# Performance work log

Measured on AMD Instinct MI355X. Metric: run time of the kernel, lower is better.

## Reference

```python
import jax, jax.numpy as jnp
import numpy as np

D_MODEL = 1024
N_HEADS = 16
N_LAYERS = 4
N_LEVELS = 8
B, T = 2, 1024
EPS = 1e-5
ADALN_K = 0.1
ADALN_C = 2.0
FMAX = float(np.finfo(np.float32).max)


def setup_inputs() -> dict:
    key = jax.random.key(0)
    ks = jax.random.split(key, 12)
    d, L = D_MODEL, N_LAYERS
    x = jax.random.normal(ks[0], (B, T, d), dtype=jnp.float32)
    # ragged lengths -> padding mask (1 valid, 0 pad), shape (b, t, 1)
    lengths = jnp.array([T, (3 * T) // 4], dtype=jnp.int32)
    m = (jnp.arange(T)[None, :] < lengths[:, None]).astype(jnp.float32)[..., None]
    l = jax.random.randint(ks[1], (B,), 0, N_LEVELS, dtype=jnp.int32)
    s = 0.02
    Wqkv = jax.random.normal(ks[2], (L, d, 3 * d), dtype=jnp.float32) * s
    Wout = jax.random.normal(ks[3], (L, d, d), dtype=jnp.float32) * s
    bout = jnp.zeros((L, d), dtype=jnp.float32)
    adaln_attn = jax.random.normal(ks[4], (L, N_LEVELS, 2 * d), dtype=jnp.float32) * s
    adaln_ffn = jax.random.normal(ks[5], (L, N_LEVELS, 2 * d), dtype=jnp.float32) * s
    W1 = jax.random.normal(ks[6], (L, d, 4 * d), dtype=jnp.float32) * s
    b1 = jnp.zeros((L, 4 * d), dtype=jnp.float32)
    W2 = jax.random.normal(ks[7], (L, 4 * d, d), dtype=jnp.float32) * s
    b2 = jnp.zeros((L, d), dtype=jnp.float32)
    return dict(x=x, m=m, l=l, Wqkv=Wqkv, Wout=Wout, bout=bout,
                adaln_attn=adaln_attn, adaln_ffn=adaln_ffn,
                W1=W1, b1=b1, W2=W2, b2=b2)


def _adaln(x, emb, l):
    # emb: (n_levels, 2d); l: (b,)
    g = emb[l][:, None, :]                      # (b, 1, 2d)
    loggamma, beta = jnp.split(g, 2, axis=-1)
    mu = jnp.mean(x, axis=-1, keepdims=True)
    var = jnp.mean((x - mu) ** 2, axis=-1, keepdims=True)
    h = (x - mu) * jax.lax.rsqrt(var + EPS)
    h = ADALN_C * (1.0 - jax.lax.stop_gradient(ADALN_K * h)) * h
    return jnp.exp(loggamma) * h + beta


def _attention(x, m, Wqkv, Wout, bout):
    b, t, d = x.shape
    h = N_HEADS
    dh = d // h
    qkv = x @ Wqkv                               # (b, t, 3d)
    q, k, v = jnp.split(qkv, 3, axis=-1)
    q = q.reshape(b, t, h, dh)
    k = k.reshape(b, t, h, dh)
    v = v.reshape(b, t, h, dh)
    e = jnp.einsum('bihd,bjhd->bijh', q, k) * (dh ** -0.5)
    kpm = m[:, None, :, :] * m[:, :, None, :]    # (b, i, j, 1)
    causal = jnp.tril(jnp.ones((t, t), dtype=kpm.dtype))[None, :, :, None]
    kpm = kpm * causal
    e = jnp.where(kpm == 0, -FMAX, e)
    a = jax.nn.softmax(e, axis=2)                # softmax over j (dim=2), matches custom softmax
    o = jnp.einsum('bijh,bjhd->bihd', a, v).reshape(b, t, d)
    o = o @ Wout + bout
    return o * m


def reference(x, m, l, Wqkv, Wout, bout, adaln_attn, adaln_ffn, W1, b1, W2, b2):
    for i in range(N_LAYERS):
        # attention sub-block (PrenormResidual with AdaLN, requires_mask=True)
        h = _adaln(x, adaln_attn[i], l) * m
        x = (x + _attention(h, m, Wqkv[i], Wout[i], bout[i])) * m
        # FFN sub-block
        h = _adaln(x, adaln_ffn[i], l) * m
        ff = jax.nn.gelu(h @ W1[i] + b1[i], approximate=False) @ W2[i] + b2[i]
        x = (x + ff) * m
    return x
```

## Files before the change

kernel.cpp:

```cpp
#include <hip/hip_runtime.h>

#define D_MODEL 1024
#define N_HEADS 16
#define DH 64
#define N_LAYERS 4
#define N_LEVELS 8
#define BB 2
#define TT 1024
#define MM (BB*TT)
#define EPSV 1e-5f

typedef float f32x4 __attribute__((ext_vector_type(4)));
typedef short bf16x8 __attribute__((ext_vector_type(8)));

__device__ __forceinline__ float bf2f(unsigned short u) {
    union { unsigned int i; float f; } c; c.i = ((unsigned int)u) << 16; return c.f;
}
__device__ __forceinline__ unsigned short f2bf(float f) {
    union { float f; unsigned int i; } c; c.f = f;
    unsigned int x = c.i;
    return (unsigned short)((x + 0x7fffu + ((x >> 16) & 1u)) >> 16);
}
__device__ __forceinline__ float cvt_in(const void* src, long long j, int isbf) {
    return isbf ? bf2f(((const unsigned short*)src)[j]) : ((const float*)src)[j];
}

__device__ __forceinline__ void gl_lds16(const unsigned short* g, unsigned short* l) {
    __builtin_amdgcn_global_load_lds(
        (const __attribute__((address_space(1))) unsigned int*)g,
        (__attribute__((address_space(3))) unsigned int*)l,
        16, 0, 0);
}

__global__ void detect_kernel(const unsigned short* __restrict__ x, int* __restrict__ flag) {
    __shared__ int cnts[256];
    int cnt = 0;
    for (int i = threadIdx.x; i < 16384; i += 256) {
        unsigned short u = x[2 * i];
        int e = (u >> 7) & 0xFF;
        if (e >= 110 && e <= 140) cnt++;
    }
    cnts[threadIdx.x] = cnt;
    __syncthreads();
    for (int s = 128; s; s >>= 1) {
        if (threadIdx.x < s) cnts[threadIdx.x] += cnts[threadIdx.x + s];
        __syncthreads();
    }
    if (threadIdx.x == 0) flag[0] = (cnts[0] > 12000) ? 1 : 0;
}

__global__ void load_f32_kernel(const void* __restrict__ src, float* __restrict__ dst,
                                const int* __restrict__ flag, int n) {
    int i = blockIdx.x * 256 + threadIdx.x;
    if (i >= n) return;
    dst[i] = cvt_in(src, i, flag[0]);
}
__global__ void load_small_kernel(const void* m_in, const void* aa, const void* af_,
                                  const void* bo, const void* b1, const void* b2,
                                  float* mf, float* embA, float* embF,
                                  float* boutf, float* b1f, float* b2f,
                                  const int* __restrict__ flag) {
    int i = blockIdx.x * 256 + threadIdx.x;
    int isbf = flag[0];
    if (i < 2048)        mf[i] = cvt_in(m_in, i, isbf);
    else if (i < 67584)  embA[i - 2048] = cvt_in(aa, i - 2048, isbf);
    else if (i < 133120) embF[i - 67584] = cvt_in(af_, i - 67584, isbf);
    else if (i < 137216) boutf[i - 133120] = cvt_in(bo, i - 133120, isbf);
    else if (i < 153600) b1f[i - 137216] = cvt_in(b1, i - 137216, isbf);
    else if (i < 157696) b2f[i - 153600] = cvt_in(b2, i - 153600, isbf);
}

__global__ __launch_bounds__(256)
void transpose_layer_kernel(const void* Wqkv, const void* Wo, const void* W1, const void* W2,
                            unsigned short* wq, unsigned short* wo,
                            unsigned short* w1, unsigned short* w2,
                            const int* __restrict__ flag,
                            long long o_qkv, long long o_o, long long o_1, long long o_2) {
    __shared__ float tile[32][33];
    int bid = blockIdx.x;
    const void* src; unsigned short* dst; long long off; int N, K, nt, kt;
    if (bid < 3072)      { int t = bid;        src = Wqkv; dst = wq; off = o_qkv; N = 3072; K = 1024; nt = t % 96;  kt = t / 96; }
    else if (bid < 4096) { int t = bid - 3072; src = Wo;   dst = wo; off = o_o;   N = 1024; K = 1024; nt = t % 32;  kt = t / 32; }
    else if (bid < 8192) { int t = bid - 4096; src = W1;   dst = w1; off = o_1;   N = 4096; K = 1024; nt = t % 128; kt = t / 128; }
    else                 { int t = bid - 8192; src = W2;   dst = w2; off = o_2;   N = 1024; K = 4096; nt = t % 32;  kt = t / 32; }
    int n0 = nt * 32, k0 = kt * 32;
    int r = threadIdx.x >> 5, c = threadIdx.x & 31;
    int isbf = flag[0];
    #pragma unroll
    for (int rr = 0; rr < 4; ++rr) {
        int k = k0 + r + rr * 8;
        tile[r + rr * 8][c] = cvt_in(src, off + (long long)k * N + n0 + c, isbf);
    }
    __syncthreads();
    #pragma unroll
    for (int rr = 0; rr < 4; ++rr) {
        int n = n0 + r + rr * 8;
        dst[(size_t)n * K + k0 + c] = f2bf(tile[c][r + rr * 8]);
    }
}

__device__ __forceinline__ void blk_sum2_256(float& a, float& b, float* red) {
    #pragma unroll
    for (int off = 32; off; off >>= 1) {
        a += __shfl_down(a, off, 64);
        b += __shfl_down(b, off, 64);
    }
    int tid = threadIdx.x;
    __syncthreads();
    if ((tid & 63) == 0) { red[tid >> 6] = a; red[4 + (tid >> 6)] = b; }
    __syncthreads();
    a = red[0] + red[1] + red[2] + red[3];
    b = red[4] + red[5] + red[6] + red[7];
}

__global__ __launch_bounds__(256)
void adaln_kernel(const float* __restrict__ x,
                  const float* __restrict__ emb,
                  const int* __restrict__ lvl,
                  const float* __restrict__ mvec,
                  unsigned short* __restrict__ h) {
    __shared__ float red[8];
    int row = blockIdx.x;
    int b = row / TT;
    int tid = threadIdx.x;
    const float* xr = x + (size_t)row * D_MODEL;
    float mval = mvec[row];
    unsigned short* hr = h + (size_t)row * D_MODEL;

    if (mval == 0.0f) {
        for (int j = tid; j < D_MODEL; j += 256) hr[j] = 0;
        return;
    }

    float s = 0.f, ss = 0.f;
    for (int j = tid; j < D_MODEL; j += 256) { float v = xr[j]; s += v; ss += v * v; }
    blk_sum2_256(s, ss, red);
    float mu = s * (1.0f / D_MODEL);
    float var = ss * (1.0f / D_MODEL) - mu * mu;
    float rstd = rsqrtf(var + EPSV);

    int lv = lvl[b];
    const float* g = emb + (size_t)lv * (2 * D_MODEL);
    for (int j = tid; j < D_MODEL; j += 256) {
        float hn = (xr[j] - mu) * rstd;
        float h2 = 2.0f * (1.0f - 0.1f * hn) * hn;
        float o = __expf(g[j]) * h2 + g[D_MODEL + j];
        hr[j] = f2bf(o * mval);
    }
}

#define EPI_STORE 0
#define EPI_GELU  1
#define EPI_RESID 2
#define EPI_PART  3

template<int MI, int NI, int WR, int WC>
__global__ __launch_bounds__(WR * WC * 64)
void gemm8_kernel(const unsigned short* __restrict__ A, int lda,
                  const unsigned short* __restrict__ BT, int ldb,
                  const float* __restrict__ bias,
                  unsigned short* __restrict__ outb,
                  const float* __restrict__ xin,
                  float* __restrict__ xout,
                  const float* __restrict__ mvec,
                  float* __restrict__ pbuf,
                  int M, int N, int K, int mode) {
    constexpr int BM = WR * MI * 16;
    constexpr int BN = WC * NI * 16;
    constexpr int NW = WR * WC;
    __shared__ __align__(16) unsigned short As[BM * 32];
    __shared__ __align__(16) unsigned short Bs[BN * 32];
    __shared__ int alive;
    int tid = threadIdx.x;
    int wave = tid >> 6;
    int lane = tid & 63;
    int quad = lane >> 4;
    int l16  = lane & 15;
    int tileM = blockIdx.y * BM;
    int tileN = blockIdx.x * BN;
    int wm = (wave % WR) * MI * 16;
    int wn = (wave / WR) * NI * 16;

    if (tid == 0) alive = 0;
    __syncthreads();
    if (tid < BM && mvec[tileM + tid] != 0.0f) alive = 1;
    __syncthreads();

    f32x4 acc[MI][NI] = {};

    if (alive) {
        long long zoff = (long long)blockIdx.z * K;
        const unsigned short* Ab = A  + zoff + (size_t)(tileM + (lane >> 2)) * lda + (lane & 3) * 8;
        const unsigned short* Bb = BT + zoff + (size_t)(tileN + (lane >> 2)) * ldb + (lane & 3) * 8;

        for (int k0 = 0; k0 < K; k0 += 32) {
            for (int st = wave; st < BM / 16; st += NW)
                gl_lds16(Ab + (size_t)st * 16 * lda + k0, &As[st * 512]);
            for (int st = wave; st < BN / 16; st += NW)
                gl_lds16(Bb + (size_t)st * 16 * ldb + k0, &Bs[st * 512]);
            __syncthreads();

            bf16x8 af[MI], bf[NI];
            #pragma unroll
            for (int mi = 0; mi < MI; ++mi)
                af[mi] = *(const bf16x8*)(&As[(wm + mi * 16 + l16) * 32 + quad * 8]);
            #pragma unroll
            for (int ni = 0; ni < NI; ++ni)
                bf[ni] = *(const bf16x8*)(&Bs[(wn + ni * 16 + l16) * 32 + quad * 8]);
            #pragma unroll
            for (int mi = 0; mi < MI; ++mi)
                #pragma unroll
                for (int ni = 0; ni < NI; ++ni)
                    acc[mi][ni] = __builtin_amdgcn_mfma_f32_16x16x32_bf16(af[mi], bf[ni], acc[mi][ni], 0, 0, 0);
            __syncthreads();
        }
    }

    #pragma unroll
    for (int mi = 0; mi < MI; ++mi)
    #pragma unroll
    for (int ni = 0; ni < NI; ++ni) {
        #pragma unroll
        for (int r = 0; r < 4; ++r) {
            int row = tileM + wm + mi * 16 + quad * 4 + r;
            int col = tileN + wn + ni * 16 + l16;
            float v = acc[mi][ni][r];
            size_t idx = (size_t)row * N + col;
            if (mode == EPI_STORE) {
                outb[idx] = f2bf(v);
            } else if (mode == EPI_GELU) {
                v += bias[col];
                float gel = 0.5f * v * (1.0f + erff(v * 0.70710678118654752f));
                outb[idx] = f2bf(gel);
            } else if (mode == EPI_RESID) {
                v += bias[col];
                xout[idx] = (xin[idx] + v) * mvec[row];
            } else {
                pbuf[(size_t)blockIdx.z * M * N + idx] = v;
            }
        }
    }
}

#define FA_DPAD 72

__global__ __launch_bounds__(256)
void fattn_split_kernel(const unsigned short* __restrict__ qkv,
                        const float* __restrict__ mvec,
                        float* __restrict__ Opart,
                        float* __restrict__ ml) {
    __shared__ __align__(16) unsigned short Qs[64 * FA_DPAD];
    __shared__ __align__(16) unsigned short Ks[64 * FA_DPAD];
    __shared__ __align__(16) unsigned short Vs[64 * FA_DPAD];
    __shared__ __align__(16) unsigned short Ps[64 * FA_DPAD];
    __shared__ int alive_s;

    int qt  = blockIdx.x;
    int hd  = blockIdx.y;
    int b   = blockIdx.z >> 1;
    int s   = blockIdx.z & 1;
    int tid = threadIdx.x;
    int wave = tid >> 6;
    int lane = tid & 63;
    int quad = lane >> 4;
    int l16  = lane & 15;

    if (tid == 0) alive_s = 0;
    __syncthreads();
    if (tid < 64 && mvec[(size_t)b * TT + qt * 64 + tid] != 0.0f) alive_s = 1;
    __syncthreads();
    bool alive = alive_s != 0;

    const unsigned short* base = qkv + (size_t)b * TT * 3072;

    f32x4 Oacc[4] = {};
    float mstate[4], lstate[4];
    #pragma unroll
    for (int r = 0; r < 4; ++r) {
        mstate[r] = alive ? -1e30f : 0.f;
        lstate[r] = alive ? 0.f : 1.f;
    }

    if (alive) {
        {
            int r = tid >> 2, c = (tid & 3) * 16;
            const unsigned short* src = base + (size_t)(qt * 64 + r) * 3072 + hd * DH + c;
            *(uint4*)(&Qs[r * FA_DPAD + c])     = *(const uint4*)(src);
            *(uint4*)(&Qs[r * FA_DPAD + c + 8]) = *(const uint4*)(src + 8);
        }
        __syncthreads();

        bf16x8 aq[2];
        #pragma unroll
        for (int cc = 0; cc < 2; ++cc)
            aq[cc] = *(const bf16x8*)(&Qs[(wave * 16 + l16) * FA_DPAD + cc * 32 + quad * 8]);

        for (int jt = s; jt <= qt; jt += 2) {
            __syncthreads();
            {
                int r = tid >> 2, c = (tid & 3) * 16;
                const unsigned short* src = base + (size_t)(jt * 64 + r) * 3072 + 1024 + hd * DH + c;
                *(uint4*)(&Ks[r * FA_DPAD + c])     = *(const uint4*)(src);
                *(uint4*)(&Ks[r * FA_DPAD + c + 8]) = *(const uint4*)(src + 8);
            }
            {
                int j = lane, c = wave * 16;
                const unsigned short* src = base + (size_t)(jt * 64 + j) * 3072 + 2048 + hd * DH + c;
                unsigned short tmp[16];
                *(uint4*)(tmp)     = *(const uint4*)(src);
                *(uint4*)(tmp + 8) = *(const uint4*)(src + 8);
                #pragma unroll
                for (int d = 0; d < 16; ++d) Vs[(c + d) * FA_DPAD + j] = tmp[d];
            }
            __syncthreads();

            f32x4 S[4] = {};
            #pragma unroll
            for (int t = 0; t < 4; ++t)
                #pragma unroll
                for (int cc = 0; cc < 2; ++cc) {
                    bf16x8 bk = *(const bf16x8*)(&Ks[(t * 16 + l16) * FA_DPAD + cc * 32 + quad * 8]);
                    S[t] = __builtin_amdgcn_mfma_f32_16x16x32_bf16(aq[cc], bk, S[t], 0, 0, 0);
                }

            int qrow0 = qt * 64 + wave * 16 + quad * 4;
            bool diag = (jt == qt);
            float mnew[4];
            #pragma unroll
            for (int r = 0; r < 4; ++r) {
                float v = -1e30f;
                #pragma unroll
                for (int t = 0; t < 4; ++t) {
                    float sv = S[t][r] * 0.125f;
                    if (diag) {
                        int j = jt * 64 + t * 16 + l16;
                        if (j > qrow0 + r) sv = -1e30f;
                    }
                    S[t][r] = sv;
                    v = fmaxf(v, sv);
                }
                v = fmaxf(v, __shfl_xor(v, 1, 64));
                v = fmaxf(v, __shfl_xor(v, 2, 64));
                v = fmaxf(v, __shfl_xor(v, 4, 64));
                v = fmaxf(v, __shfl_xor(v, 8, 64));
                mnew[r] = fmaxf(mstate[r], v);
            }

            #pragma unroll
            for (int r = 0; r < 4; ++r) {
                float rs = 0.f;
                #pragma unroll
                for (int t = 0; t < 4; ++t) {
                    float p = __expf(S[t][r] - mnew[r]);
                    rs += p;
                    Ps[(wave * 16 + quad * 4 + r) * FA_DPAD + t * 16 + l16] = f2bf(p);
                }
                rs += __shfl_xor(rs, 1, 64);
                rs += __shfl_xor(rs, 2, 64);
                rs += __shfl_xor(rs, 4, 64);
                rs += __shfl_xor(rs, 8, 64);
                float alpha = __expf(mstate[r] - mnew[r]);
                lstate[r] = alpha * lstate[r] + rs;
                mstate[r] = mnew[r];
                #pragma unroll
                for (int t = 0; t < 4; ++t) Oacc[t][r] *= alpha;
            }

            #pragma unroll
            for (int cc = 0; cc < 2; ++cc) {
                bf16x8 ap = *(const bf16x8*)(&Ps[(wave * 16 + l16) * FA_DPAD + cc * 32 + quad * 8]);
                #pragma unroll
                for (int t = 0; t < 4; ++t) {
                    bf16x8 bv = *(const bf16x8*)(&Vs[(t * 16 + l16) * FA_DPAD + cc * 32 + quad * 8]);
                    Oacc[t] = __builtin_amdgcn_mfma_f32_16x16x32_bf16(ap, bv, Oacc[t], 0, 0, 0);
                }
            }
        }
    }

    #pragma unroll
    for (int r = 0; r < 4; ++r) {
        int qi = qt * 64 + wave * 16 + quad * 4 + r;
        size_t row = (size_t)b * TT + qi;
        float* orow = Opart + (size_t)s * MM * D_MODEL + row * D_MODEL + hd * DH;
        #pragma unroll
        for (int t = 0; t < 4; ++t)
            orow[t * 16 + l16] = Oacc[t][r];
        if (l16 == 0) {
            float* mlp = ml + (((size_t)s * MM + row) * N_HEADS + hd) * 2;
            mlp[0] = mstate[r];
            mlp[1] = lstate[r];
        }
    }
}

__global__ void attn_merge_kernel(const float* __restrict__ Opart,
                                  const float* __restrict__ ml,
                                  unsigned short* __restrict__ ob) {
    int i = blockIdx.x * 256 + threadIdx.x;
    int row = i >> 10;
    int hd  = (i >> 6) & 15;
    const float* ml0 = ml + (((size_t)row) * N_HEADS + hd) * 2;
    const float* ml1 = ml + (((size_t)MM + row) * N_HEADS + hd) * 2;
    float m0 = ml0[0], l0 = ml0[1];
    float m1 = ml1[0], l1 = ml1[1];
    float M = fmaxf(m0, m1);
    float w0 = __expf(m0 - M), w1 = __expf(m1 - M);
    float den = w0 * l0 + w1 * l1;
    float num = w0 * Opart[i] + w1 * Opart[(size_t)MM * D_MODEL + i];
    ob[i] = f2bf(num / den);
}

__global__ void combine2_kernel(float* __restrict__ xf,
                                const float* __restrict__ pbuf,
                                const float* __restrict__ bias,
                                const float* __restrict__ mvec,
                                void* __restrict__ outp,
                                const int* __restrict__ flag, int n) {
    int i = blockIdx.x * 256 + threadIdx.x;
    if (i >= n) return;
    int row = i >> 10, col = i & 1023;
    float v = (xf[i] + pbuf[i] + pbuf[n + i] + bias[col]) * mvec[row];
    xf[i] = v;
    if (outp) {
        if (flag[0]) ((unsigned short*)outp)[i] = f2bf(v);
        else         ((float*)outp)[i] = v;
    }
}

#define MB (1048576u)
#define WS_FLAG   0u
#define WS_MF     4096u
#define WS_EMBA   (WS_MF + 8192u)
#define WS_EMBF   (WS_EMBA + 262144u)
#define WS_BOUT   (WS_EMBF + 262144u)
#define WS_B1     (WS_BOUT + 16384u)
#define WS_B2     (WS_B1 + 65536u)
#define WS_XF     (1u*MB)
#define WS_H      (9u*MB)
#define WS_QKV    (13u*MB)
#define WS_OB     (25u*MB)
#define WS_PART   (9u*MB)
#define WS_ML     (9u*MB)
#define WS_FF1    (29u*MB)
#define WS_OPART  (29u*MB)
#define WS_WQKV   (45u*MB)
#define WS_WOUT   (51u*MB)
#define WS_W1     (53u*MB)
#define WS_W2     (61u*MB)

extern "C" void kernel_launch(void* const* d_in, const int* in_sizes, int n_in,
                              void* d_out, int out_size, void* d_ws, size_t ws_size,
                              hipStream_t stream) {
    const void* x_in  = d_in[0];
    const void* m_in  = d_in[1];
    const int*  l_in  = (const int*)d_in[2];
    const void* Wqkv  = d_in[3];
    const void* Wout  = d_in[4];
    const void* boutp = d_in[5];
    const void* ada_a = d_in[6];
    const void* ada_f = d_in[7];
    const void* W1    = d_in[8];
    const void* b1    = d_in[9];
    const void* W2    = d_in[10];
    const void* b2    = d_in[11];

    char* ws = (char*)d_ws;
    int*            flag = (int*)(ws + WS_FLAG);
    float*          mf   = (float*)(ws + WS_MF);
    float*          embA = (float*)(ws + WS_EMBA);
    float*          embF = (float*)(ws + WS_EMBF);
    float*          boutf= (float*)(ws + WS_BOUT);
    float*          b1f  = (float*)(ws + WS_B1);
    float*          b2f  = (float*)(ws + WS_B2);
    float*          xf   = (float*)(ws + WS_XF);
    unsigned short* h    = (unsigned short*)(ws + WS_H);
    unsigned short* qkv  = (unsigned short*)(ws + WS_QKV);
    unsigned short* ob   = (unsigned short*)(ws + WS_OB);
    float*          part = (float*)(ws + WS_PART);
    float*          mlb  = (float*)(ws + WS_ML);
    float*          opart= (float*)(ws + WS_OPART);
    unsigned short* ff1  = (unsigned short*)(ws + WS_FF1);
    unsigned short* wqkvt= (unsigned short*)(ws + WS_WQKV);
    unsigned short* woutt= (unsigned short*)(ws + WS_WOUT);
    unsigned short* w1t  = (unsigned short*)(ws + WS_W1);
    unsigned short* w2t  = (unsigned short*)(ws + WS_W2);

    const int n = MM * D_MODEL;

    detect_kernel<<<1, 256, 0, stream>>>((const unsigned short*)x_in, flag);
    load_f32_kernel<<<n / 256, 256, 0, stream>>>(x_in, xf, flag, n);
    load_small_kernel<<<(157696 + 255) / 256, 256, 0, stream>>>(
        m_in, ada_a, ada_f, boutp, b1, b2, mf, embA, embF, boutf, b1f, b2f, flag);

    const long long nqkv = (long long)D_MODEL * 3 * D_MODEL;
    const long long nsq  = (long long)D_MODEL * D_MODEL;
    const long long nw1  = (long long)D_MODEL * 4 * D_MODEL;

    for (int i = 0; i < N_LAYERS; ++i) {
        transpose_layer_kernel<<<12288, 256, 0, stream>>>(
            Wqkv, Wout, W1, W2, wqkvt, woutt, w1t, w2t, flag,
            i * nqkv, i * nsq, i * nw1, i * nw1);

        adaln_kernel<<<MM, 256, 0, stream>>>(xf, embA + (size_t)i * N_LEVELS * 2 * D_MODEL, l_in, mf, h);
        gemm8_kernel<4,2,2,2><<<dim3(3072 / 64, MM / 128), 256, 0, stream>>>(
            h, 1024, wqkvt, 1024, nullptr, qkv, nullptr, nullptr, mf, nullptr,
            MM, 3072, 1024, EPI_STORE);
        fattn_split_kernel<<<dim3(TT / 64, N_HEADS, BB * 2), 256, 0, stream>>>(qkv, mf, opart, mlb);
        attn_merge_kernel<<<n / 256, 256, 0, stream>>>(opart, mlb, ob);
        gemm8_kernel<2,2,4,2><<<dim3(1024 / 64, MM / 128), 512, 0, stream>>>(
            ob, 1024, woutt, 1024, boutf + (size_t)i * D_MODEL, nullptr, xf, xf, mf, nullptr,
            MM, 1024, 1024, EPI_RESID);
        adaln_kernel<<<MM, 256, 0, stream>>>(xf, embF + (size_t)i * N_LEVELS * 2 * D_MODEL, l_in, mf, h);
        gemm8_kernel<4,2,2,4><<<dim3(4096 / 128, MM / 128), 512, 0, stream>>>(
            h, 1024, w1t, 1024, b1f + (size_t)i * 4 * D_MODEL, ff1, nullptr, nullptr, mf, nullptr,
            MM, 4096, 1024, EPI_GELU);
        gemm8_kernel<2,2,4,2><<<dim3(1024 / 64, MM / 128, 2), 512, 0, stream>>>(
            ff1, 4096, w2t, 4096, nullptr, nullptr, nullptr, nullptr, mf, part,
            MM, 1024, 2048, EPI_PART);
        combine2_kernel<<<n / 256, 256, 0, stream>>>(
            xf, part, b2f + (size_t)i * D_MODEL, mf,
            (i == N_LAYERS - 1) ? d_out : nullptr, flag, n);
    }
}
```

Baseline: 999.4 us.

## Double-buffer GEMM LDS tiles and vectorize AdaLN row processing

```diff
diff --git a/kernel.cpp b/kernel.cpp
--- a/kernel.cpp
+++ b/kernel.cpp
@@ -12,6 +12,7 @@
 
 typedef float f32x4 __attribute__((ext_vector_type(4)));
 typedef short bf16x8 __attribute__((ext_vector_type(8)));
+typedef unsigned short u16x4 __attribute__((ext_vector_type(4)));
 
 __device__ __forceinline__ float bf2f(unsigned short u) {
     union { unsigned int i; float f; } c; c.i = ((unsigned int)u) << 16; return c.f;
@@ -128,12 +129,14 @@
     unsigned short* hr = h + (size_t)row * D_MODEL;
 
     if (mval == 0.0f) {
-        for (int j = tid; j < D_MODEL; j += 256) hr[j] = 0;
+        u16x4 z = (u16x4)0;
+        *(u16x4*)(hr + 4 * tid) = z;
         return;
     }
 
-    float s = 0.f, ss = 0.f;
-    for (int j = tid; j < D_MODEL; j += 256) { float v = xr[j]; s += v; ss += v * v; }
+    f32x4 xv = *(const f32x4*)(xr + 4 * tid);
+    float s = xv[0] + xv[1] + xv[2] + xv[3];
+    float ss = xv[0]*xv[0] + xv[1]*xv[1] + xv[2]*xv[2] + xv[3]*xv[3];
     blk_sum2_256(s, ss, red);
     float mu = s * (1.0f / D_MODEL);
     float var = ss * (1.0f / D_MODEL) - mu * mu;
@@ -141,12 +144,17 @@
 
     int lv = lvl[b];
     const float* g = emb + (size_t)lv * (2 * D_MODEL);
-    for (int j = tid; j < D_MODEL; j += 256) {
-        float hn = (xr[j] - mu) * rstd;
+    f32x4 lg = *(const f32x4*)(g + 4 * tid);
+    f32x4 lb = *(const f32x4*)(g + D_MODEL + 4 * tid);
+    u16x4 r;
+    #pragma unroll
+    for (int c = 0; c < 4; ++c) {
+        float hn = (xv[c] - mu) * rstd;
         float h2 = 2.0f * (1.0f - 0.1f * hn) * hn;
-        float o = __expf(g[j]) * h2 + g[D_MODEL + j];
-        hr[j] = f2bf(o * mval);
-    }
+        float o = __expf(lg[c]) * h2 + lb[c];
+        r[c] = f2bf(o * mval);
+    }
+    *(u16x4*)(hr + 4 * tid) = r;
 }
 
 #define EPI_STORE 0
@@ -168,8 +176,8 @@
     constexpr int BM = WR * MI * 16;
     constexpr int BN = WC * NI * 16;
     constexpr int NW = WR * WC;
-    __shared__ __align__(16) unsigned short As[BM * 32];
-    __shared__ __align__(16) unsigned short Bs[BN * 32];
+    __shared__ __align__(16) unsigned short As[2][BM * 32];
+    __shared__ __align__(16) unsigned short Bs[2][BN * 32];
     __shared__ int alive;
     int tid = threadIdx.x;
     int wave = tid >> 6;
@@ -193,26 +201,36 @@
         const unsigned short* Ab = A  + zoff + (size_t)(tileM + (lane >> 2)) * lda + (lane & 3) * 8;
         const unsigned short* Bb = BT + zoff + (size_t)(tileN + (lane >> 2)) * ldb + (lane & 3) * 8;
 
+        for (int st = wave; st < BM / 16; st += NW)
+            gl_lds16(Ab + (size_t)st * 16 * lda, &As[0][st * 512]);
+        for (int st = wave; st < BN / 16; st += NW)
+            gl_lds16(Bb + (size_t)st * 16 * ldb, &Bs[0][st * 512]);
+        __syncthreads();
+
+        int cur = 0;
         for (int k0 = 0; k0 < K; k0 += 32) {
-            for (int st = wave; st < BM / 16; st += NW)
-                gl_lds16(Ab + (size_t)st * 16 * lda + k0, &As[st * 512]);
-            for (int st = wave; st < BN / 16; st += NW)
-                gl_lds16(Bb + (size_t)st * 16 * ldb + k0, &Bs[st * 512]);
-            __syncthreads();
+            if (k0 + 32 < K) {
+                for (int st = wave; st < BM / 16; st += NW)
+                    gl_lds16(Ab + (size_t)st * 16 * lda + k0 + 32, &As[cur ^ 1][st * 512]);
+                for (int st = wave; st < BN / 16; st += NW)
+                    gl_lds16(Bb + (size_t)st * 16 * ldb + k0 + 32, &Bs[cur ^ 1][st * 512]);
+            }
 
             bf16x8 af[MI], bf[NI];
             #pragma unroll
             for (int mi = 0; mi < MI; ++mi)
-                af[mi] = *(const bf16x8*)(&As[(wm + mi * 16 + l16) * 32 + quad * 8]);
+                af[mi] = *(const bf16x8*)(&As[cur][(wm + mi * 16 + l16) * 32 + quad * 8]);
             #pragma unroll
             for (int ni = 0; ni < NI; ++ni)
-                bf[ni] = *(const bf16x8*)(&Bs[(wn + ni * 16 + l16) * 32 + quad * 8]);
+                bf[ni] = *(const bf16x8*)(&Bs[cur][(wn + ni * 16 + l16) * 32 + quad * 8]);
             #pragma unroll
             for (int mi = 0; mi < MI; ++mi)
                 #pragma unroll
                 for (int ni = 0; ni < NI; ++ni)
                     acc[mi][ni] = __builtin_amdgcn_mfma_f32_16x16x32_bf16(af[mi], bf[ni], acc[mi][ni], 0, 0, 0);
+
             __syncthreads();
+            cur ^= 1;
         }
     }
 
```

After: 972.1 us. -2.7%, faster.
